# Performance work log

Measured on AMD Instinct MI355X. Metric: run time of the kernel, lower is better.

Reference implementation:

```python
import jax, jax.numpy as jnp
import numpy as np

K = 4096  # n_selections: real nodes selected per virtual node


def setup_inputs() -> dict:
    key = jax.random.key(0)
    ks = jax.random.split(key, 7)
    N, n_in, n_virtual = 800000, 128, 2
    d = n_in * n_virtual
    x = jax.random.normal(ks[0], (N, n_in), dtype=jnp.float32)
    W_fr = jax.random.normal(ks[1], (n_in, n_virtual), dtype=jnp.float32) * (1.0 / np.sqrt(n_in))
    b_fr = jnp.zeros((n_virtual,), dtype=jnp.float32)
    W1 = jax.random.normal(ks[2], (d, d), dtype=jnp.float32) * (1.0 / np.sqrt(d))
    b1 = jnp.zeros((d,), dtype=jnp.float32)
    W2 = jax.random.normal(ks[3], (d, d), dtype=jnp.float32) * (1.0 / np.sqrt(d))
    b2 = jnp.zeros((d,), dtype=jnp.float32)
    return {"x": x, "W_fr": W_fr, "b_fr": b_fr, "W1": W1, "b1": b1,
            "W2": W2, "b2": b2, "n_batches": 8}


def reference(x, W_fr, b_fr, W1, b1, W2, b2, n_batches):
    N, n_in = x.shape
    V = W_fr.shape[1]
    R = N // n_batches
    xb = x.reshape(n_batches, R, n_in)                      # [B,R,F]
    scores = jnp.einsum('brf,fv->brv', xb, W_fr) + b_fr     # [B,R,V]
    # SIMPLE sampler: select top-K real nodes per virtual node (hard mask)
    _, idx = jax.lax.top_k(scores.transpose(0, 2, 1), K)    # [B,V,K]
    b_ix = jnp.arange(n_batches)[:, None, None]
    v_ix = jnp.arange(V)[None, :, None]
    mask = jnp.zeros((n_batches, V, R), dtype=bool).at[b_ix, v_ix, idx].set(True)  # [B,V,R]
    # masked mean aggregation real -> virtual (exactly K selected per (b,v))
    virt = jnp.einsum('bvr,brf->bvf', mask.astype(x.dtype), xb) / K  # [B,V,F]
    # virtual-virtual MLP on flattened virtual features
    h = virt.reshape(n_batches, V * n_in)
    h = jax.nn.relu(h @ W1 + b1) @ W2 + b2
    virt_upd = h.reshape(n_batches, V, n_in)                # [B,V,F]
    # sequential in-place scatter update per virtual node (order matters)
    out = xb
    for v in range(V):
        m = mask[:, v, :, None]                             # [B,R,1]
        out = jnp.where(m, (out + virt_upd[:, v:v + 1, :]) * 0.5, out)
    return out.reshape(N, n_in)
```

## Files before the change

### kernel.cpp

```cpp
#include <hip/hip_runtime.h>

#define N_IN   128
#define DD     256
#define KSEL   4096
#define NBATCH 8
#define NGROUP 16
#define HSLOTS 4
#define K1_CPB 250
#define K1_ROWS 400
#define CCH    8
#define CSPAN  12500
#define SUBCAP 4096u
#define CAPG   (CCH*4096)
#define WCH    13
#define VCH    64
#define USLICE 16

__device__ __forceinline__ unsigned keyOf(float s){
    unsigned b = __float_as_uint(s);
    return (b & 0x80000000u) ? ~b : (b | 0x80000000u);
}

__device__ __forceinline__ float4 blend4(float4 o, float4 u){
    o.x = (o.x + u.x)*0.5f; o.y = (o.y + u.y)*0.5f;
    o.z = (o.z + u.z)*0.5f; o.w = (o.w + u.w)*0.5f;
    return o;
}

__global__ __launch_bounds__(256) void zero_kernel(uint4* __restrict__ p, int n16){
    const int i = blockIdx.x * 256 + threadIdx.x;
    if (i < n16) p[i] = uint4{0u,0u,0u,0u};
}

__global__ __launch_bounds__(256) void scores_hist_copy_kernel(
        const float* __restrict__ x, const float* __restrict__ W_fr,
        const float* __restrict__ b_fr, unsigned* __restrict__ keys,
        unsigned* __restrict__ gHist, float* __restrict__ out, int N, int R)
{
    const int b   = blockIdx.x / K1_CPB;
    const int c   = blockIdx.x % K1_CPB;
    const int rbase = b * R + c * K1_ROWS;
    const int tid = threadIdx.x;
    const int wave = tid >> 6, lane = tid & 63;

    __shared__ unsigned h0[2048], h1[2048];
    for (int i = tid; i < 2048; i += 256){ h0[i] = 0u; h1[i] = 0u; }
    __syncthreads();

    const int f = 4 * (lane & 31);
    const float w00 = W_fr[(f+0)*2+0], w01 = W_fr[(f+0)*2+1];
    const float w10 = W_fr[(f+1)*2+0], w11 = W_fr[(f+1)*2+1];
    const float w20 = W_fr[(f+2)*2+0], w21 = W_fr[(f+2)*2+1];
    const float w30 = W_fr[(f+3)*2+0], w31 = W_fr[(f+3)*2+1];
    const float bf0 = b_fr[0], bf1 = b_fr[1];

    for (int it = 0; it < K1_ROWS/8; ++it){
        const int r0 = rbase + it*8 + wave*2;
        const size_t base = (size_t)r0 * N_IN + 4*lane;
        const float4 xv = *reinterpret_cast<const float4*>(x + base);
        *reinterpret_cast<float4*>(out + base) = xv;
        double p0 = (double)xv.x*w00 + (double)xv.y*w10 + (double)xv.z*w20 + (double)xv.w*w30;
        double p1 = (double)xv.x*w01 + (double)xv.y*w11 + (double)xv.z*w21 + (double)xv.w*w31;
        #pragma unroll
        for (int off = 16; off; off >>= 1){
            p0 += __shfl_xor(p0, off, 32);
            p1 += __shfl_xor(p1, off, 32);
        }
        const unsigned k0 = keyOf((float)(p0 + bf0));
        const unsigned k1 = keyOf((float)(p1 + bf1));
        const int r = r0 + (lane >> 5);
        if ((lane & 31) == 0){ keys[r]     = k0; atomicAdd(&h0[k0 >> 21], 1u); }
        if ((lane & 31) == 1){ keys[N + r] = k1; atomicAdd(&h1[k1 >> 21], 1u); }
    }
    __syncthreads();
    const int slot = c & (HSLOTS-1);
    unsigned* gh0 = gHist + ((size_t)(2*b)   * HSLOTS + slot) * 2048;
    unsigned* gh1 = gHist + ((size_t)(2*b+1) * HSLOTS + slot) * 2048;
    for (int bin = tid; bin < 2048; bin += 256){
        const unsigned s0 = h0[bin], s1 = h1[bin];
        if (s0) atomicAdd(&gh0[bin], s0);
        if (s1) atomicAdd(&gh1[bin], s1);
    }
}

__global__ __launch_bounds__(1024) void collect_kernel(
        const unsigned* __restrict__ keys, const unsigned* __restrict__ gHist,
        unsigned* __restrict__ gCandCnt, unsigned long long* __restrict__ cand,
        int N, int R)
{
    const int g = blockIdx.x >> 3, ch = blockIdx.x & 7;
    const int b = g >> 1, v = g & 1;
    const unsigned* kk = keys + (size_t)v * N + (size_t)b * R;
    const int tid = threadIdx.x, wv = tid >> 6, lane = tid & 63;

    __shared__ unsigned lh[2048];
    __shared__ unsigned coarse[32];
    __shared__ unsigned sB1;
    __shared__ unsigned wcnt[16];
    __shared__ unsigned sLoc;

    {
        const unsigned* gh = gHist + (size_t)g * HSLOTS * 2048;
        for (int bin = tid; bin < 2048; bin += 1024){
            unsigned ss = 0;
            #pragma unroll
            for (int sl = 0; sl < HSLOTS; ++sl) ss += gh[sl*2048 + bin];
            lh[bin] = ss;
        }
        __syncthreads();
        if (tid < 32){ unsigned ss = 0; for (int j = 0; j < 64; ++j) ss += lh[tid*64+j]; coarse[tid] = ss; }
        __syncthreads();
        if (tid == 0){
            unsigned kneed = KSEL, cum = 0; int cb = 31;
            for (; cb > 0; --cb){ if (cum + coarse[cb] >= kneed) break; cum += coarse[cb]; }
            int bin = cb*64 + 63;
            for (; bin > cb*64; --bin){ if (cum + lh[bin] >= kneed) break; cum += lh[bin]; }
            sB1 = (unsigned)bin; sLoc = 0u;
        }
        __syncthreads();
    }
    const unsigned B1 = sB1;

    unsigned long long* cd = cand + (size_t)g * CAPG + (size_t)ch * 4096;
    const int lo = ch * CSPAN, hi = min(R, lo + CSPAN);
    for (int i0 = lo; i0 < hi; i0 += 1024){
        const int i = i0 + tid;
        const bool pred = (i < hi) && ((kk[i] >> 21) == B1);
        const unsigned u = pred ? kk[i] : 0u;
        unsigned long long m = __ballot(pred);
        if (lane == 0) wcnt[wv] = (unsigned)__popcll(m);
        __syncthreads();
        unsigned pre = sLoc, tot = 0;
        #pragma unroll
        for (int w = 0; w < 16; ++w){ const unsigned cc = wcnt[w]; if (w < wv) pre += cc; tot += cc; }
        if (pred){
            const unsigned p = pre + (unsigned)__popcll(m & ((1ULL << lane) - 1ULL));
            if (p < SUBCAP) cd[p] = ((unsigned long long)u << 32) | (unsigned)i;
        }
        __syncthreads();
        if (tid == 0) sLoc += tot;
        __syncthreads();
    }
    if (tid == 0) gCandCnt[g*CCH + ch] = min(sLoc, SUBCAP);
}

__global__ __launch_bounds__(1024) void select2_kernel(
        const unsigned* __restrict__ gHist, const unsigned long long* __restrict__ cand,
        const unsigned* __restrict__ gCandCnt, unsigned* __restrict__ gParams)
{
    const int g = blockIdx.x;
    const int tid = threadIdx.x;

    __shared__ unsigned lh[2048];
    __shared__ unsigned coarse[32];
    __shared__ unsigned sB[2];
    __shared__ unsigned nccs[CCH];

    {
        const unsigned* gh = gHist + (size_t)g * HSLOTS * 2048;
        for (int bin = tid; bin < 2048; bin += 1024){
            unsigned ss = 0;
            #pragma unroll
            for (int sl = 0; sl < HSLOTS; ++sl) ss += gh[sl*2048 + bin];
            lh[bin] = ss;
        }
        __syncthreads();
        if (tid < 32){ unsigned ss = 0; for (int j = 0; j < 64; ++j) ss += lh[tid*64+j]; coarse[tid] = ss; }
        __syncthreads();
        if (tid == 0){
            unsigned kneed = KSEL, cum = 0; int cb = 31;
            for (; cb > 0; --cb){ if (cum + coarse[cb] >= kneed) break; cum += coarse[cb]; }
            int bin = cb*64 + 63;
            for (; bin > cb*64; --bin){ if (cum + lh[bin] >= kneed) break; cum += lh[bin]; }
            sB[0] = (unsigned)bin; sB[1] = kneed - cum;
        }
        __syncthreads();
    }
    const unsigned B1 = sB[0], kneed1 = sB[1];
    if (tid < CCH) nccs[tid] = gCandCnt[g*CCH + tid];
    __syncthreads();
    const unsigned long long* cd0 = cand + (size_t)g * CAPG;

    for (int i = tid; i < 2048; i += 1024) lh[i] = 0u;
    __syncthreads();
    for (int c2 = 0; c2 < CCH; ++c2){
        const int n = (int)nccs[c2];
        const unsigned long long* cdp = cd0 + (size_t)c2*4096;
        for (int i = tid; i < n; i += 1024)
            atomicAdd(&lh[((unsigned)(cdp[i] >> 32) >> 10) & 0x7FFu], 1u);
    }
    __syncthreads();
    if (tid < 32){ unsigned ss = 0; for (int j = 0; j < 64; ++j) ss += lh[tid*64+j]; coarse[tid] = ss; }
    __syncthreads();
    if (tid == 0){
        unsigned kneed = kneed1, cum = 0; int cb = 31;
        for (; cb > 0; --cb){ if (cum + coarse[cb] >= kneed) break; cum += coarse[cb]; }
        int bin = cb*64 + 63;
        for (; bin > cb*64; --bin){ if (cum + lh[bin] >= kneed) break; cum += lh[bin]; }
        sB[0] = (unsigned)bin; sB[1] = kneed - cum;
    }
    __syncthreads();
    const unsigned B2 = sB[0], kneed2 = sB[1];
    const unsigned top22 = (B1 << 11) | B2;
    __syncthreads();

    for (int i = tid; i < 1024; i += 1024) lh[i] = 0u;
    __syncthreads();
    for (int c2 = 0; c2 < CCH; ++c2){
        const int n = (int)nccs[c2];
        const unsigned long long* cdp = cd0 + (size_t)c2*4096;
        for (int i = tid; i < n; i += 1024){
            const unsigned u = (unsigned)(cdp[i] >> 32);
            if ((u >> 10) == top22) atomicAdd(&lh[u & 0x3FFu], 1u);
        }
    }
    __syncthreads();
    if (tid < 32){ unsigned ss = 0; for (int j = 0; j < 32; ++j) ss += lh[tid*32+j]; coarse[tid] = ss; }
    __syncthreads();
    if (tid == 0){
        unsigned kneed = kneed2, cum = 0; int cb = 31;
        for (; cb > 0; --cb){ if (cum + coarse[cb] >= kneed) break; cum += coarse[cb]; }
        int bin = cb*32 + 31;
        for (; bin > cb*32; --bin){ if (cum + lh[bin] >= kneed) break; cum += lh[bin]; }
        sB[0] = (unsigned)bin; sB[1] = kneed - cum;
    }
    __syncthreads();
    const unsigned B3 = sB[0], take_eq = sB[1];
    const unsigned utar = (B1 << 21) | (B2 << 10) | B3;
    __syncthreads();

    for (int i = tid; i < 1024; i += 1024) lh[i] = 0u;
    __syncthreads();
    for (int c2 = 0; c2 < CCH; ++c2){
        const int n = (int)nccs[c2];
        const unsigned long long* cdp = cd0 + (size_t)c2*4096;
        for (int i = tid; i < n; i += 1024){
            const unsigned long long e = cdp[i];
            if ((unsigned)(e >> 32) == utar) atomicAdd(&lh[((unsigned)e) >> 7], 1u);
        }
    }
    __syncthreads();
    if (tid < 32){ unsigned ss = 0; for (int j = 0; j < 32; ++j) ss += lh[tid*32+j]; coarse[tid] = ss; }
    __syncthreads();
    if (tid == 0){
        unsigned need = take_eq, cum = 0; int cb = 0;
        for (; cb < 31; ++cb){ if (cum + coarse[cb] >= need) break; cum += coarse[cb]; }
        int bin = cb*32;
        for (; bin < cb*32+31; ++bin){ if (cum + lh[bin] >= need) break; cum += lh[bin]; }
        sB[0] = (unsigned)bin; sB[1] = need - cum;
    }
    __syncthreads();
    const unsigned cb7 = sB[0], rem = sB[1];
    __syncthreads();

    if (tid < 128) lh[tid] = 0u;
    __syncthreads();
    for (int c2 = 0; c2 < CCH; ++c2){
        const int n = (int)nccs[c2];
        const unsigned long long* cdp = cd0 + (size_t)c2*4096;
        for (int i = tid; i < n; i += 1024){
            const unsigned long long e = cdp[i];
            const unsigned ix = (unsigned)e;
            if ((unsigned)(e >> 32) == utar && (ix >> 7) == cb7) atomicAdd(&lh[ix & 127], 1u);
        }
    }
    __syncthreads();
    if (tid == 0){
        unsigned need = rem, cum = 0; int p = 0;
        for (; p < 127; ++p){ if (cum + lh[p] >= need) break; cum += lh[p]; }
        gParams[g*8+2] = utar;
        gParams[g*8+3] = cb7*128 + (unsigned)p;
    }
}

__global__ __launch_bounds__(1024) void write_kernel(
        const unsigned* __restrict__ keys, const unsigned* __restrict__ gParams,
        int* __restrict__ lists, unsigned* __restrict__ gListCnt, int N, int R)
{
    const int g = blockIdx.x / WCH, c = blockIdx.x % WCH;
    const int b = g >> 1, v = g & 1;
    const unsigned* kk = keys + (size_t)v * N + (size_t)b * R;
    int* lst = lists + g * KSEL;
    const unsigned utar = gParams[g*8+2];
    const int T = (int)gParams[g*8+3];
    const int tid = threadIdx.x, wave = tid >> 6, lane = tid & 63;
    const int i0 = c * 8192;

    bool pr[8];
    #pragma unroll
    for (int j = 0; j < 8; ++j){
        const int i = i0 + j*1024 + tid;
        const unsigned u = (i < R) ? kk[i] : 0u;
        pr[j] = (i < R) && (u > utar || (u == utar && i <= T));
    }
    __shared__ unsigned wc[8][16];
    __shared__ unsigned ec[8][16];
    __shared__ unsigned sBase;
    #pragma unroll
    for (int j = 0; j < 8; ++j){
        unsigned long long m = __ballot(pr[j]);
        if (lane == 0) wc[j][wave] = (unsigned)__popcll(m);
    }
    __syncthreads();
    if (tid == 0){
        unsigned run = 0;
        for (int j = 0; j < 8; ++j)
            for (int w = 0; w < 16; ++w){ ec[j][w] = run; run += wc[j][w]; }
        sBase = run ? atomicAdd(&gListCnt[g*16], run) : 0u;
    }
    __syncthreads();
    const unsigned base = sBase;
    #pragma unroll
    for (int j = 0; j < 8; ++j){
        unsigned long long m = __ballot(pr[j]);
        if (pr[j])
            lst[base + ec[j][wave] + (unsigned)__popcll(m & ((1ULL << lane) - 1ULL))] = i0 + j*1024 + tid;
    }
}

__global__ __launch_bounds__(256) void virt_partial_kernel(
        const float* __restrict__ x, const int* __restrict__ lists,
        double* __restrict__ part, int R)
{
    const int g = blockIdx.x >> 6;
    const int m = blockIdx.x & 63;
    const int b = g >> 1;
    const int tid = threadIdx.x, wave = tid >> 6, lane = tid & 63;
    const int* lst = lists + g * KSEL + m * 64;
    int idxs[16];
    #pragma unroll
    for (int e = 0; e < 16; ++e) idxs[e] = lst[e*4 + wave];
    double a0 = 0.0, a1 = 0.0;
    #pragma unroll
    for (int e = 0; e < 16; ++e){
        const float2 xv = *reinterpret_cast<const float2*>(
            x + ((size_t)b * R + idxs[e]) * N_IN + 2*lane);
        a0 += xv.x; a1 += xv.y;
    }
    __shared__ double pp[4][128];
    pp[wave][2*lane]   = a0;
    pp[wave][2*lane+1] = a1;
    __syncthreads();
    if (tid < 128){
        double s = pp[0][tid] + pp[1][tid] + pp[2][tid] + pp[3][tid];
        part[(size_t)(g*VCH + m) * N_IN + tid] = s;
    }
}

__global__ __launch_bounds__(256) void update_mlp_kernel(
        const float* __restrict__ x, const unsigned* __restrict__ keys,
        const int* __restrict__ lists, const double* __restrict__ part,
        const unsigned* __restrict__ gParams,
        const float* __restrict__ W1, const float* __restrict__ b1,
        const float* __restrict__ W2, const float* __restrict__ b2,
        float* __restrict__ out, int N, int R)
{
    const int g = blockIdx.x >> 4, sl = blockIdx.x & (USLICE-1);
    const int b = g >> 1, v = g & 1;
    const int tid = threadIdx.x;

    __shared__ __align__(16) float inv[DD];
    __shared__ __align__(16) float h1s[DD];
    __shared__ __align__(16) float uu[DD];

    {
        const int g2 = b*2 + (tid >> 7);
        const int fcol = tid & 127;
        double ssum = 0.0;
        for (int cc = 0; cc < VCH; ++cc) ssum += part[((size_t)g2 * VCH + cc) * N_IN + fcol];
        inv[tid] = (float)(ssum / (double)KSEL);
    }
    __syncthreads();
    {
        double q0=0, q1=0, q2=0, q3=0;
        for (int i = 0; i < DD; i += 4){
            q0 += (double)inv[i+0] * (double)W1[(i+0)*DD + tid];
            q1 += (double)inv[i+1] * (double)W1[(i+1)*DD + tid];
            q2 += (double)inv[i+2] * (double)W1[(i+2)*DD + tid];
            q3 += (double)inv[i+3] * (double)W1[(i+3)*DD + tid];
        }
        h1s[tid] = fmaxf((float)(((q0+q1)+(q2+q3)) + (double)b1[tid]), 0.0f);
    }
    __syncthreads();
    {
        double q0=0, q1=0, q2=0, q3=0;
        for (int i = 0; i < DD; i += 4){
            q0 += (double)h1s[i+0] * (double)W2[(i+0)*DD + tid];
            q1 += (double)h1s[i+1] * (double)W2[(i+1)*DD + tid];
            q2 += (double)h1s[i+2] * (double)W2[(i+2)*DD + tid];
            q3 += (double)h1s[i+3] * (double)W2[(i+3)*DD + tid];
        }
        uu[tid] = (float)(((q0+q1)+(q2+q3)) + (double)b2[tid]);
    }
    __syncthreads();

    const int wave = tid >> 6, lane = tid & 63;
    const int half = lane >> 5;
    const int c4 = (lane & 31) * 4;
    const int* lst = lists + g * KSEL + sl * (KSEL/USLICE);
    const unsigned* k0p = keys + (size_t)b * R;
    const unsigned* k1p = keys + (size_t)N + (size_t)b * R;
    const unsigned utar0 = gParams[(b*2+0)*8+2]; const int T0  = (int)gParams[(b*2+0)*8+3];
    const unsigned utar1 = gParams[(b*2+1)*8+2]; const int T1v = (int)gParams[(b*2+1)*8+3];
    const float4 u0 = *reinterpret_cast<const float4*>(&uu[c4]);
    const float4 u1 = *reinterpret_cast<const float4*>(&uu[128 + c4]);
    const size_t rowBase = (size_t)b * R;

    for (int e = wave*2 + half; e < KSEL/USLICE; e += 8){
        const int row = lst[e];
        if (v == 1){
            const unsigned uk0 = k0p[row];
            if (uk0 > utar0 || (uk0 == utar0 && row <= T0)) continue;
        }
        const size_t base = (rowBase + row) * N_IN + c4;
        float4 o = *reinterpret_cast<const float4*>(x + base);
        if (v == 0){
            o = blend4(o, u0);
            const unsigned uk1 = k1p[row];
            if (uk1 > utar1 || (uk1 == utar1 && row <= T1v)) o = blend4(o, u1);
        } else {
            o = blend4(o, u1);
        }
        *reinterpret_cast<float4*>(out + base) = o;
    }
}

extern "C" void kernel_launch(void* const* d_in, const int* in_sizes, int n_in_cnt,
                              void* d_out, int out_size, void* d_ws, size_t ws_size,
                              hipStream_t stream)
{
    const float* x    = (const float*)d_in[0];
    const float* W_fr = (const float*)d_in[1];
    const float* b_fr = (const float*)d_in[2];
    const float* W1   = (const float*)d_in[3];
    const float* b1   = (const float*)d_in[4];
    const float* W2   = (const float*)d_in[5];
    const float* b2   = (const float*)d_in[6];
    float* out = (float*)d_out;
    const int N = in_sizes[0] / N_IN;
    const int R = N / NBATCH;

    char* ws = (char*)d_ws;
    size_t off = 0;
    auto alloc = [&](size_t bytes) -> void* {
        void* p = ws + off;
        off = (off + bytes + 255) & ~(size_t)255;
        return p;
    };
    int*                lists   = (int*)               alloc((size_t)NGROUP * KSEL * 4);
    double*             part    = (double*)            alloc((size_t)NGROUP * VCH * N_IN * 8);
    unsigned long long* cand    = (unsigned long long*)alloc((size_t)NGROUP * CAPG * 8);
    unsigned*           keys    = (unsigned*)          alloc((size_t)2 * N * 4);
    unsigned*           gParams = (unsigned*)          alloc((size_t)NGROUP * 8 * 4);
    unsigned*           gCandCnt= (unsigned*)          alloc((size_t)NGROUP * CCH * 4);

    const size_t zrUints = 16*16 + (size_t)NGROUP * HSLOTS * 2048;
    unsigned* zr = (unsigned*)alloc(zrUints * 4);
    unsigned* gListCnt = zr;
    unsigned* gHist    = zr + 16*16;

    const int n16 = (int)((zrUints * 4 + 15) / 16);
    zero_kernel<<<dim3((n16 + 255)/256), dim3(256), 0, stream>>>((uint4*)zr, n16);
    scores_hist_copy_kernel<<<dim3(NBATCH*K1_CPB), dim3(256), 0, stream>>>(
        x, W_fr, b_fr, keys, gHist, out, N, R);
    collect_kernel<<<dim3(NGROUP*CCH), dim3(1024), 0, stream>>>(
        keys, gHist, gCandCnt, cand, N, R);
    select2_kernel<<<dim3(NGROUP), dim3(1024), 0, stream>>>(
        gHist, cand, gCandCnt, gParams);
    write_kernel<<<dim3(NGROUP*WCH), dim3(1024), 0, stream>>>(
        keys, gParams, lists, gListCnt, N, R);
    virt_partial_kernel<<<dim3(NGROUP*VCH), dim3(256), 0, stream>>>(
        x, lists, part, R);
    update_mlp_kernel<<<dim3(NGROUP*USLICE), dim3(256), 0, stream>>>(
        x, keys, lists, part, gParams, W1, b1, W2, b2, out, N, R);
}
```

Before: 300.0 us.

## Fuse collect with select via last-block-done, and fuse list write with gather

Merges the candidate collection and the second-level selection into one kernel. The last-finishing chunk block per group, detected through an atomic done counter and thread fences, performs the refinement. It also folds the virtual-feature partial-sum gather into the list-writing kernel, so each block sums x rows for the indices it just wrote and stores one partial per chunk. This removes two kernel launches and their inter-kernel gaps. The cost is that the refine step now runs in a single tail block per group, and the gather is done by fewer, larger blocks with a shared-memory double reduction.

New measurement: 344.6 us. 14.9% more time.

```diff
diff --git a/kernel.cpp b/kernel.cpp
--- a/kernel.cpp
+++ b/kernel.cpp
@@ -13,7 +13,6 @@
 #define SUBCAP 4096u
 #define CAPG   (CCH*4096)
 #define WCH    13
-#define VCH    64
 #define USLICE 16
 
 __device__ __forceinline__ unsigned keyOf(float s){
@@ -83,9 +82,10 @@
     }
 }
 
-__global__ __launch_bounds__(1024) void collect_kernel(
+__global__ __launch_bounds__(1024) void collect_refine_kernel(
         const unsigned* __restrict__ keys, const unsigned* __restrict__ gHist,
         unsigned* __restrict__ gCandCnt, unsigned long long* __restrict__ cand,
+        unsigned* __restrict__ gParams, unsigned* __restrict__ gDone,
         int N, int R)
 {
     const int g = blockIdx.x >> 3, ch = blockIdx.x & 7;
@@ -95,66 +95,11 @@
 
     __shared__ unsigned lh[2048];
     __shared__ unsigned coarse[32];
-    __shared__ unsigned sB1;
+    __shared__ unsigned sB[2];
     __shared__ unsigned wcnt[16];
     __shared__ unsigned sLoc;
-
-    {
-        const unsigned* gh = gHist + (size_t)g * HSLOTS * 2048;
-        for (int bin = tid; bin < 2048; bin += 1024){
-            unsigned ss = 0;
-            #pragma unroll
-            for (int sl = 0; sl < HSLOTS; ++sl) ss += gh[sl*2048 + bin];
-            lh[bin] = ss;
-        }
-        __syncthreads();
-        if (tid < 32){ unsigned ss = 0; for (int j = 0; j < 64; ++j) ss += lh[tid*64+j]; coarse[tid] = ss; }
-        __syncthreads();
-        if (tid == 0){
-            unsigned kneed = KSEL, cum = 0; int cb = 31;
-            for (; cb > 0; --cb){ if (cum + coarse[cb] >= kneed) break; cum += coarse[cb]; }
-            int bin = cb*64 + 63;
-            for (; bin > cb*64; --bin){ if (cum + lh[bin] >= kneed) break; cum += lh[bin]; }
-            sB1 = (unsigned)bin; sLoc = 0u;
-        }
-        __syncthreads();
-    }
-    const unsigned B1 = sB1;
-
-    unsigned long long* cd = cand + (size_t)g * CAPG + (size_t)ch * 4096;
-    const int lo = ch * CSPAN, hi = min(R, lo + CSPAN);
-    for (int i0 = lo; i0 < hi; i0 += 1024){
-        const int i = i0 + tid;
-        const bool pred = (i < hi) && ((kk[i] >> 21) == B1);
-        const unsigned u = pred ? kk[i] : 0u;
-        unsigned long long m = __ballot(pred);
-        if (lane == 0) wcnt[wv] = (unsigned)__popcll(m);
-        __syncthreads();
-        unsigned pre = sLoc, tot = 0;
-        #pragma unroll
-        for (int w = 0; w < 16; ++w){ const unsigned cc = wcnt[w]; if (w < wv) pre += cc; tot += cc; }
-        if (pred){
-            const unsigned p = pre + (unsigned)__popcll(m & ((1ULL << lane) - 1ULL));
-            if (p < SUBCAP) cd[p] = ((unsigned long long)u << 32) | (unsigned)i;
-        }
-        __syncthreads();
-        if (tid == 0) sLoc += tot;
-        __syncthreads();
-    }
-    if (tid == 0) gCandCnt[g*CCH + ch] = min(sLoc, SUBCAP);
-}
-
-__global__ __launch_bounds__(1024) void select2_kernel(
-        const unsigned* __restrict__ gHist, const unsigned long long* __restrict__ cand,
-        const unsigned* __restrict__ gCandCnt, unsigned* __restrict__ gParams)
-{
-    const int g = blockIdx.x;
-    const int tid = threadIdx.x;
-
-    __shared__ unsigned lh[2048];
-    __shared__ unsigned coarse[32];
-    __shared__ unsigned sB[2];
     __shared__ unsigned nccs[CCH];
+    __shared__ unsigned sOld;
 
     {
         const unsigned* gh = gHist + (size_t)g * HSLOTS * 2048;
@@ -173,10 +118,42 @@
             int bin = cb*64 + 63;
             for (; bin > cb*64; --bin){ if (cum + lh[bin] >= kneed) break; cum += lh[bin]; }
             sB[0] = (unsigned)bin; sB[1] = kneed - cum;
+            sLoc = 0u;
         }
         __syncthreads();
     }
     const unsigned B1 = sB[0], kneed1 = sB[1];
+
+    {
+        unsigned long long* cd = cand + (size_t)g * CAPG + (size_t)ch * 4096;
+        const int lo = ch * CSPAN, hi = min(R, lo + CSPAN);
+        for (int i0 = lo; i0 < hi; i0 += 1024){
+            const int i = i0 + tid;
+            const bool pred = (i < hi) && ((kk[i] >> 21) == B1);
+            const unsigned u = pred ? kk[i] : 0u;
+            unsigned long long m = __ballot(pred);
+            if (lane == 0) wcnt[wv] = (unsigned)__popcll(m);
+            __syncthreads();
+            unsigned pre = sLoc, tot = 0;
+            #pragma unroll
+            for (int w = 0; w < 16; ++w){ const unsigned cc = wcnt[w]; if (w < wv) pre += cc; tot += cc; }
+            if (pred){
+                const unsigned p = pre + (unsigned)__popcll(m & ((1ULL << lane) - 1ULL));
+                if (p < SUBCAP) cd[p] = ((unsigned long long)u << 32) | (unsigned)i;
+            }
+            __syncthreads();
+            if (tid == 0) sLoc += tot;
+            __syncthreads();
+        }
+        if (tid == 0) gCandCnt[g*CCH + ch] = min(sLoc, SUBCAP);
+    }
+
+    __threadfence();
+    if (tid == 0) sOld = atomicAdd(&gDone[g*16], 1u);
+    __syncthreads();
+    if (sOld != CCH-1) return;
+    __threadfence();
+
     if (tid < CCH) nccs[tid] = gCandCnt[g*CCH + tid];
     __syncthreads();
     const unsigned long long* cd0 = cand + (size_t)g * CAPG;
@@ -273,9 +250,11 @@
     }
 }
 
-__global__ __launch_bounds__(1024) void write_kernel(
+__global__ __launch_bounds__(1024) void write_gather_kernel(
         const unsigned* __restrict__ keys, const unsigned* __restrict__ gParams,
-        int* __restrict__ lists, unsigned* __restrict__ gListCnt, int N, int R)
+        const float* __restrict__ x, int* __restrict__ lists,
+        unsigned* __restrict__ gListCnt, double* __restrict__ part,
+        int N, int R)
 {
     const int g = blockIdx.x / WCH, c = blockIdx.x % WCH;
     const int b = g >> 1, v = g & 1;
@@ -296,6 +275,7 @@
     __shared__ unsigned wc[8][16];
     __shared__ unsigned ec[8][16];
     __shared__ unsigned sBase;
+    __shared__ double red[32][128];
     #pragma unroll
     for (int j = 0; j < 8; ++j){
         unsigned long long m = __ballot(pr[j]);
@@ -307,43 +287,44 @@
         for (int j = 0; j < 8; ++j)
             for (int w = 0; w < 16; ++w){ ec[j][w] = run; run += wc[j][w]; }
         sBase = run ? atomicAdd(&gListCnt[g*16], run) : 0u;
+        wc[0][0] = run;
     }
     __syncthreads();
     const unsigned base = sBase;
+    const unsigned run = wc[0][0];
     #pragma unroll
     for (int j = 0; j < 8; ++j){
         unsigned long long m = __ballot(pr[j]);
         if (pr[j])
             lst[base + ec[j][wave] + (unsigned)__popcll(m & ((1ULL << lane) - 1ULL))] = i0 + j*1024 + tid;
     }
-}
-
-__global__ __launch_bounds__(256) void virt_partial_kernel(
-        const float* __restrict__ x, const int* __restrict__ lists,
-        double* __restrict__ part, int R)
-{
-    const int g = blockIdx.x >> 6;
-    const int m = blockIdx.x & 63;
-    const int b = g >> 1;
-    const int tid = threadIdx.x, wave = tid >> 6, lane = tid & 63;
-    const int* lst = lists + g * KSEL + m * 64;
-    int idxs[16];
+    __syncthreads();
+
+    const float* xb = x + (size_t)b * R * N_IN;
+    const int slot = tid >> 5;
+    const int c4 = (tid & 31) * 4;
+    double a0 = 0.0, a1 = 0.0, a2 = 0.0, a3 = 0.0;
+    for (unsigned rr = slot; rr < run; rr += 32){
+        const float4 xv = *reinterpret_cast<const float4*>(
+            xb + (size_t)lst[base + rr] * N_IN + c4);
+        a0 += xv.x; a1 += xv.y; a2 += xv.z; a3 += xv.w;
+    }
+    red[slot][c4+0] = a0; red[slot][c4+1] = a1;
+    red[slot][c4+2] = a2; red[slot][c4+3] = a3;
+    __syncthreads();
     #pragma unroll
-    for (int e = 0; e < 16; ++e) idxs[e] = lst[e*4 + wave];
-    double a0 = 0.0, a1 = 0.0;
-    #pragma unroll
-    for (int e = 0; e < 16; ++e){
-        const float2 xv = *reinterpret_cast<const float2*>(
-            x + ((size_t)b * R + idxs[e]) * N_IN + 2*lane);
-        a0 += xv.x; a1 += xv.y;
-    }
-    __shared__ double pp[4][128];
-    pp[wave][2*lane]   = a0;
-    pp[wave][2*lane+1] = a1;
-    __syncthreads();
-    if (tid < 128){
-        double s = pp[0][tid] + pp[1][tid] + pp[2][tid] + pp[3][tid];
-        part[(size_t)(g*VCH + m) * N_IN + tid] = s;
+    for (int st = 16; st >= 1; st >>= 1){
+        if (slot < st){
+            #pragma unroll
+            for (int k = 0; k < 4; ++k)
+                red[slot][c4+k] += red[slot+st][c4+k];
+        }
+        __syncthreads();
+    }
+    if (slot == 0){
+        double* pp = part + ((size_t)g * WCH + c) * N_IN;
+        pp[c4+0] = red[0][c4+0]; pp[c4+1] = red[0][c4+1];
+        pp[c4+2] = red[0][c4+2]; pp[c4+3] = red[0][c4+3];
     }
 }
 
@@ -367,7 +348,7 @@
         const int g2 = b*2 + (tid >> 7);
         const int fcol = tid & 127;
         double ssum = 0.0;
-        for (int cc = 0; cc < VCH; ++cc) ssum += part[((size_t)g2 * VCH + cc) * N_IN + fcol];
+        for (int cc = 0; cc < WCH; ++cc) ssum += part[((size_t)g2 * WCH + cc) * N_IN + fcol];
         inv[tid] = (float)(ssum / (double)KSEL);
     }
     __syncthreads();
@@ -448,29 +429,26 @@
         return p;
     };
     int*                lists   = (int*)               alloc((size_t)NGROUP * KSEL * 4);
-    double*             part    = (double*)            alloc((size_t)NGROUP * VCH * N_IN * 8);
+    double*             part    = (double*)            alloc((size_t)NGROUP * WCH * N_IN * 8);
     unsigned long long* cand    = (unsigned long long*)alloc((size_t)NGROUP * CAPG * 8);
     unsigned*           keys    = (unsigned*)          alloc((size_t)2 * N * 4);
     unsigned*           gParams = (unsigned*)          alloc((size_t)NGROUP * 8 * 4);
     unsigned*           gCandCnt= (unsigned*)          alloc((size_t)NGROUP * CCH * 4);
 
-    const size_t zrUints = 16*16 + (size_t)NGROUP * HSLOTS * 2048;
+    const size_t zrUints = 16*16 + 16*16 + (size_t)NGROUP * HSLOTS * 2048;
     unsigned* zr = (unsigned*)alloc(zrUints * 4);
-    unsigned* gListCnt = zr;
-    unsigned* gHist    = zr + 16*16;
+    unsigned* gDone    = zr;
+    unsigned* gListCnt = zr + 16*16;
+    unsigned* gHist    = zr + 16*16 + 16*16;
 
     const int n16 = (int)((zrUints * 4 + 15) / 16);
     zero_kernel<<<dim3((n16 + 255)/256), dim3(256), 0, stream>>>((uint4*)zr, n16);
     scores_hist_copy_kernel<<<dim3(NBATCH*K1_CPB), dim3(256), 0, stream>>>(
         x, W_fr, b_fr, keys, gHist, out, N, R);
-    collect_kernel<<<dim3(NGROUP*CCH), dim3(1024), 0, stream>>>(
-        keys, gHist, gCandCnt, cand, N, R);
-    select2_kernel<<<dim3(NGROUP), dim3(1024), 0, stream>>>(
-        gHist, cand, gCandCnt, gParams);
-    write_kernel<<<dim3(NGROUP*WCH), dim3(1024), 0, stream>>>(
-        keys, gParams, lists, gListCnt, N, R);
-    virt_partial_kernel<<<dim3(NGROUP*VCH), dim3(256), 0, stream>>>(
-        x, lists, part, R);
+    collect_refine_kernel<<<dim3(NGROUP*CCH), dim3(1024), 0, stream>>>(
+        keys, gHist, gCandCnt, cand, gParams, gDone, N, R);
+    write_gather_kernel<<<dim3(NGROUP*WCH), dim3(1024), 0, stream>>>(
+        keys, gParams, x, lists, gListCnt, part, N, R);
     update_mlp_kernel<<<dim3(NGROUP*USLICE), dim3(256), 0, stream>>>(
         x, keys, lists, part, gParams, W1, b1, W2, b2, out, N, R);
 }
```
